# Kernel tuning notes

Measured on AMD Instinct MI355X. Metric: run time of the kernel, lower is better.

## Reference

```python
import jax, jax.numpy as jnp
import numpy as np

B, T, D = 4, 1024, 1024
H, DH = 8, 128           # heads, dim_head = dim // heads
E, FF = 8, 2048          # num_experts, expert hidden_dim
LN_EPS = 1e-5


def setup_inputs() -> dict:
    key = jax.random.key(0)
    ks = jax.random.split(key, 20)
    s = 0.02
    inp = {
        'v': jax.random.normal(ks[0], (B, T, D), jnp.float32),
        'k': jax.random.normal(ks[1], (B, T, D), jnp.float32),
        'q': jax.random.normal(ks[2], (B, T, D), jnp.float32),
        'noise': jax.random.normal(ks[3], (B * T, E), jnp.float32),
        # LayerNorm params (norm_v, norm_k, norm_q, norm_moe, moe output norm)
        'g_v': jnp.ones((D,)), 'b_v': jnp.zeros((D,)),
        'g_k': jnp.ones((D,)), 'b_k': jnp.zeros((D,)),
        'g_q': jnp.ones((D,)), 'b_q': jnp.zeros((D,)),
        'g_moe': jnp.ones((D,)), 'b_moe': jnp.zeros((D,)),
        'g_out': jnp.ones((D,)), 'b_out': jnp.zeros((D,)),
        # LinearAttention projections (q/k/v have no bias, out_proj has bias)
        'Wq': jax.random.normal(ks[4], (D, H * DH), jnp.float32) * s,
        'Wk': jax.random.normal(ks[5], (D, H * DH), jnp.float32) * s,
        'Wv': jax.random.normal(ks[6], (D, H * DH), jnp.float32) * s,
        'Wo': jax.random.normal(ks[7], (H * DH, D), jnp.float32) * s,
        'bo': jnp.zeros((D,)),
        # Router
        'Wr': jax.random.normal(ks[8], (D, E), jnp.float32) * s,
        'br': jnp.zeros((E,)),
        # Experts (stacked): dim -> FF -> dim
        'W1': jax.random.normal(ks[9], (E, D, FF), jnp.float32) * s,
        'b1': jnp.zeros((E, FF)),
        'W2': jax.random.normal(ks[10], (E, FF, D), jnp.float32) * s,
        'b2': jnp.zeros((E, D)),
        'top_k': 2,
    }
    return inp


def _ln(x, g, b):
    mu = x.mean(-1, keepdims=True)
    x0 = x - mu
    var = (x0 * x0).mean(-1, keepdims=True)
    return x0 * jax.lax.rsqrt(var + LN_EPS) * g + b


def reference(v, k, q, noise, g_v, b_v, g_k, b_k, g_q, b_q, g_moe, b_moe,
              g_out, b_out, Wq, Wk, Wv, Wo, bo, Wr, br, W1, b1, W2, b2, top_k):
    # --- LinearAttention over pre-normed v,k,q ---
    qh = jnp.einsum('btd,de->bte', _ln(q, g_q, b_q), Wq).reshape(B, T, H, DH)
    kh = jnp.einsum('btd,de->bte', _ln(k, g_k, b_k), Wk).reshape(B, T, H, DH)
    vh = jnp.einsum('btd,de->bte', _ln(v, g_v, b_v), Wv).reshape(B, T, H, DH)
    qf = jax.nn.elu(qh) + 1.0
    kf = jax.nn.elu(kh) + 1.0
    kv = jnp.einsum('bthd,bthe->bhde', kf, vh)          # [B,H,DH,DH]
    out = jnp.einsum('bthd,bhde->bthe', qf, kv)         # [B,T,H,DH]
    k_sum = kf.sum(axis=1) + 1e-6                       # [B,H,DH]
    denom = jnp.einsum('bthd,bhd->bth', qf, k_sum)[..., None]
    out = out / denom
    attn_out = jnp.einsum('bte,ed->btd', out.reshape(B, T, H * DH), Wo) + bo

    q_res = q + attn_out

    # --- MoEBlock: noisy top-k routing + expert MLPs + residual + LayerNorm ---
    x = _ln(q_res, g_moe, b_moe)
    xf = x.reshape(B * T, D)
    logits = xf @ Wr + br + noise * 0.1                 # noisy gating (randn/10)
    scores = jax.nn.softmax(logits, axis=-1)
    topk_s, topk_i = jax.lax.top_k(scores, top_k)       # [N,K]
    combine = (jax.nn.one_hot(topk_i, E, dtype=scores.dtype) * topk_s[..., None]).sum(1)  # [N,E]
    h = jax.nn.gelu(jnp.einsum('nd,edh->enh', xf, W1) + b1[:, None, :], approximate=False)
    eo = jnp.einsum('enh,ehd->end', h, W2) + b2[:, None, :]
    moe = jnp.einsum('end,ne->nd', eo, combine)         # weighted combine == masked dispatch
    moe_out = _ln(moe.reshape(B, T, D) + x, g_out, b_out)

    return q_res + moe_out
```

## Files before the change

### kernel.cpp

```cpp
#include <hip/hip_runtime.h>
#include <math.h>

typedef __attribute__((ext_vector_type(8))) short short8;
typedef __attribute__((ext_vector_type(4))) float f32x4;

#define LN_EPS 1e-5f

__device__ __forceinline__ float bf2f(unsigned short u) {
  unsigned int x = ((unsigned int)u) << 16;
  float f;
  __builtin_memcpy(&f, &x, 4);
  return f;
}
__device__ __forceinline__ unsigned short f2bf(float f) {
  unsigned int x;
  __builtin_memcpy(&x, &f, 4);
  x += 0x7fffu + ((x >> 16) & 1u);
  return (unsigned short)(x >> 16);
}

__device__ __forceinline__ void gload16(const void* g, void* l) {
  __builtin_amdgcn_global_load_lds(
      (__attribute__((address_space(1))) void*)(void*)g,
      (__attribute__((address_space(3))) void*)l, 16, 0, 0);
}

__device__ __forceinline__ void xcd_swizzle(int& bx, int& by) {
  const int nx = gridDim.x;
  const int nwg = nx * gridDim.y;
  const int orig = blockIdx.y * nx + blockIdx.x;
  const int cpx = nwg >> 3;
  const int lid = (orig & 7) * cpx + (orig >> 3);
  bx = lid % nx;
  by = lid / nx;
}

__device__ __forceinline__ void blockReduce2(float& a, float& b, float* s8) {
#pragma unroll
  for (int off = 32; off > 0; off >>= 1) {
    a += __shfl_down(a, off);
    b += __shfl_down(b, off);
  }
  const int w = threadIdx.x >> 6;
  if ((threadIdx.x & 63) == 0) { s8[w] = a; s8[4 + w] = b; }
  __syncthreads();
  a = s8[0] + s8[1] + s8[2] + s8[3];
  b = s8[4] + s8[5] + s8[6] + s8[7];
}

__global__ __launch_bounds__(256) void ln3_kernel(
    const float* __restrict__ q, const float* __restrict__ k, const float* __restrict__ v,
    const float* __restrict__ gq, const float* __restrict__ bq,
    const float* __restrict__ gk, const float* __restrict__ bk,
    const float* __restrict__ gv, const float* __restrict__ bv,
    unsigned short* __restrict__ oq, unsigned short* __restrict__ ok,
    unsigned short* __restrict__ ov) {
  __shared__ float s8[8];
  const int row = blockIdx.x, which = blockIdx.y;
  const float* x = which == 0 ? q : which == 1 ? k : v;
  const float* g = which == 0 ? gq : which == 1 ? gk : gv;
  const float* b = which == 0 ? bq : which == 1 ? bk : bv;
  unsigned short* o = which == 0 ? oq : which == 1 ? ok : ov;
  const float4 xv = ((const float4*)(x + (size_t)row * 1024))[threadIdx.x];
  float s = xv.x + xv.y + xv.z + xv.w;
  float s2 = xv.x * xv.x + xv.y * xv.y + xv.z * xv.z + xv.w * xv.w;
  blockReduce2(s, s2, s8);
  const float mu = s * (1.f / 1024.f);
  const float rs = rsqrtf(s2 * (1.f / 1024.f) - mu * mu + LN_EPS);
  const int c = threadIdx.x * 4;
  const float y[4] = {xv.x, xv.y, xv.z, xv.w};
#pragma unroll
  for (int j = 0; j < 4; ++j)
    o[(size_t)row * 1024 + c + j] = f2bf((y[j] - mu) * rs * g[c + j] + b[c + j]);
}

__global__ __launch_bounds__(256) void ln_moe_router_kernel(
    const float* __restrict__ qres, const float* __restrict__ g, const float* __restrict__ b,
    const float* __restrict__ Wr, const float* __restrict__ br,
    const float* __restrict__ noise,
    float* __restrict__ xf, unsigned short* __restrict__ xb,
    int* __restrict__ pick, float* __restrict__ pw) {
  __shared__ float s8[8];
  __shared__ float sacc[32];
  const int row = blockIdx.x;
  const float4 xv = ((const float4*)(qres + (size_t)row * 1024))[threadIdx.x];
  float s = xv.x + xv.y + xv.z + xv.w;
  float s2 = xv.x * xv.x + xv.y * xv.y + xv.z * xv.z + xv.w * xv.w;
  blockReduce2(s, s2, s8);
  const float mu = s * (1.f / 1024.f);
  const float rs = rsqrtf(s2 * (1.f / 1024.f) - mu * mu + LN_EPS);
  const int c = threadIdx.x * 4;
  const float yin[4] = {xv.x, xv.y, xv.z, xv.w};
  float y[4];
#pragma unroll
  for (int j = 0; j < 4; ++j) {
    y[j] = (yin[j] - mu) * rs * g[c + j] + b[c + j];
    xf[(size_t)row * 1024 + c + j] = y[j];
    xb[(size_t)row * 1024 + c + j] = f2bf(y[j]);
  }
  float acc[8] = {};
  const float4* wrv = (const float4*)(Wr + (size_t)c * 8);
#pragma unroll
  for (int j = 0; j < 4; ++j) {
    const float4 w0 = wrv[j * 2], w1 = wrv[j * 2 + 1];
    acc[0] += y[j] * w0.x; acc[1] += y[j] * w0.y;
    acc[2] += y[j] * w0.z; acc[3] += y[j] * w0.w;
    acc[4] += y[j] * w1.x; acc[5] += y[j] * w1.y;
    acc[6] += y[j] * w1.z; acc[7] += y[j] * w1.w;
  }
#pragma unroll
  for (int off = 32; off > 0; off >>= 1)
#pragma unroll
    for (int e = 0; e < 8; ++e) acc[e] += __shfl_down(acc[e], off);
  const int w = threadIdx.x >> 6;
  if ((threadIdx.x & 63) == 0)
#pragma unroll
    for (int e = 0; e < 8; ++e) sacc[w * 8 + e] = acc[e];
  __syncthreads();
  if (threadIdx.x == 0) {
    float lg[8], mx = -1e30f;
#pragma unroll
    for (int e = 0; e < 8; ++e) {
      lg[e] = sacc[e] + sacc[8 + e] + sacc[16 + e] + sacc[24 + e] + br[e] +
              0.1f * noise[(size_t)row * 8 + e];
      mx = fmaxf(mx, lg[e]);
    }
    float ssum = 0.f;
#pragma unroll
    for (int e = 0; e < 8; ++e) { lg[e] = expf(lg[e] - mx); ssum += lg[e]; }
    const float inv = 1.f / ssum;
#pragma unroll
    for (int e = 0; e < 8; ++e) lg[e] *= inv;
    int i1 = -1, i2 = -1;
    float m1 = -1.f, m2 = -1.f;
#pragma unroll
    for (int e = 0; e < 8; ++e) {
      if (lg[e] > m1) { m2 = m1; i2 = i1; m1 = lg[e]; i1 = e; }
      else if (lg[e] > m2) { m2 = lg[e]; i2 = e; }
    }
    pick[row * 2] = i1; pick[row * 2 + 1] = i2;
    pw[row * 2] = m1;  pw[row * 2 + 1] = m2;
  }
}

__global__ __launch_bounds__(1024) void route_build_kernel(
    const int* __restrict__ pick, const float* __restrict__ pw,
    int* __restrict__ seg, int* __restrict__ tok, float* __restrict__ wgt,
    int* __restrict__ slt) {
  __shared__ int cnt[8];
  __shared__ int segs[9];
  __shared__ int cur[8];
  const int tid = threadIdx.x;
  if (tid < 8) { cnt[tid] = 0; cur[tid] = 0; }
  __syncthreads();
  for (int i = tid; i < 8192; i += 1024) atomicAdd(&cnt[pick[i]], 1);
  __syncthreads();
  if (tid == 0) {
    int o = 0;
    for (int e = 0; e < 8; ++e) { segs[e] = o; o += (cnt[e] + 127) & ~127; }
    segs[8] = o;
  }
  __syncthreads();
  for (int i = tid; i < 9216; i += 1024) tok[i] = -1;
  if (tid < 9) seg[tid] = segs[tid];
  __syncthreads();
  for (int i = tid; i < 8192; i += 1024) {
    const int n = i >> 1, sl = i & 1;
    const int e = pick[i];
    const int p = atomicAdd(&cur[e], 1);
    const int gr = segs[e] + p;
    tok[gr] = n;
    wgt[gr] = pw[i];
    slt[gr] = sl;
  }
}

__global__ __launch_bounds__(256) void final_kernel(
    const unsigned short* __restrict__ eoSb, const float* __restrict__ xf,
    const float* __restrict__ qres, const float* __restrict__ g,
    const float* __restrict__ b, float* __restrict__ out) {
  __shared__ float s8[8];
  const int row = blockIdx.x;
  const size_t SLOT = (size_t)4096 * 1024;
  const short8 m0v = *(const short8*)(eoSb + (size_t)row * 1024 + threadIdx.x * 4 -
                                      (threadIdx.x * 4 & 7) + ((threadIdx.x & 1) ? 0 : 0));
  const unsigned short* p0 = eoSb + (size_t)row * 1024 + threadIdx.x * 4;
  const unsigned short* p1 = eoSb + SLOT + (size_t)row * 1024 + threadIdx.x * 4;
  const float4 xv = ((const float4*)(xf + (size_t)row * 1024))[threadIdx.x];
  float y[4];
#pragma unroll
  for (int j = 0; j < 4; ++j) y[j] = bf2f(p0[j]) + bf2f(p1[j]);
  y[0] += xv.x; y[1] += xv.y; y[2] += xv.z; y[3] += xv.w;
  float s = y[0] + y[1] + y[2] + y[3];
  float s2 = y[0] * y[0] + y[1] * y[1] + y[2] * y[2] + y[3] * y[3];
  blockReduce2(s, s2, s8);
  const float mu = s * (1.f / 1024.f);
  const float rs = rsqrtf(s2 * (1.f / 1024.f) - mu * mu + LN_EPS);
  const int c = threadIdx.x * 4;
#pragma unroll
  for (int j = 0; j < 4; ++j) {
    const size_t idx = (size_t)row * 1024 + c + j;
    out[idx] = qres[idx] + (y[j] - mu) * rs * g[c + j] + b[c + j];
  }
}

__global__ __launch_bounds__(256) void transposeB_kernel(
    const float* const* __restrict__ ins, unsigned short* const* __restrict__ outs,
    int R, int C) {
  __shared__ float t[32][33];
  const float* inz = ins[blockIdx.z];
  unsigned short* outz = outs[blockIdx.z];
  const int bx = blockIdx.x, by = blockIdx.y;
  const int tx = threadIdx.x & 31, ty = threadIdx.x >> 5;
#pragma unroll
  for (int i = 0; i < 32; i += 8)
    t[ty + i][tx] = inz[(size_t)(by * 32 + ty + i) * C + bx * 32 + tx];
  __syncthreads();
#pragma unroll
  for (int i = 0; i < 32; i += 8)
    outz[(size_t)(bx * 32 + ty + i) * R + by * 32 + tx] = f2bf(t[tx][ty + i]);
}

__global__ __launch_bounds__(256) void transpose8_kernel(
    const float* __restrict__ in, unsigned short* __restrict__ out, int R, int C) {
  __shared__ float t[32][33];
  const float* inz = in + (size_t)blockIdx.z * R * C;
  unsigned short* outz = out + (size_t)blockIdx.z * R * C;
  const int bx = blockIdx.x, by = blockIdx.y;
  const int tx = threadIdx.x & 31, ty = threadIdx.x >> 5;
#pragma unroll
  for (int i = 0; i < 32; i += 8)
    t[ty + i][tx] = inz[(size_t)(by * 32 + ty + i) * C + bx * 32 + tx];
  __syncthreads();
#pragma unroll
  for (int i = 0; i < 32; i += 8)
    outz[(size_t)(bx * 32 + ty + i) * R + by * 32 + tx] = f2bf(t[tx][ty + i]);
}

#define GEMM_STAGE(buf, k0, KD)                                              \
  gload16(gA0 + (k0), lA + (buf) * 4096);                                    \
  gload16(gA1 + (k0), lA + (buf) * 4096 + 16 * 32);                          \
  gload16(gB + (k0), lB + (buf) * 4096);                                     \
  gload16(gB + (size_t)16 * (KD) + (k0), lB + (buf) * 4096 + 16 * 32);

#define GEMM_COMPUTE(buf)                                                    \
  {                                                                          \
    const unsigned short* sA = &As[buf][0];                                  \
    const unsigned short* sB = &Bs[buf][0];                                  \
    short8 af[4], bfr[4];                                                    \
    _Pragma("unroll") for (int m = 0; m < 4; ++m)                            \
        af[m] = *(const short8*)&sA[(arow + m * 16) * 32 + kk];              \
    _Pragma("unroll") for (int n = 0; n < 4; ++n)                            \
        bfr[n] = *(const short8*)&sB[(brow + n * 16) * 32 + kk];             \
    _Pragma("unroll") for (int m = 0; m < 4; ++m)                            \
      _Pragma("unroll") for (int n = 0; n < 4; ++n)                          \
        acc[m][n] = __builtin_amdgcn_mfma_f32_16x16x32_bf16(                 \
            a f[m], bfr[n], acc[m][n], 0, 0, 0);                             \
  }
#undef GEMM_COMPUTE
#define GEMM_COMPUTE(buf)                                                    \
  {                                                                          \
    const unsigned short* sA = &As[buf][0];                                  \
    const unsigned short* sB = &Bs[buf][0];                                  \
    short8 af[4], bfr[4];                                                    \
    _Pragma("unroll") for (int m = 0; m < 4; ++m)                            \
        af[m] = *(const short8*)&sA[(arow + m * 16) * 32 + kk];              \
    _Pragma("unroll") for (int n = 0; n < 4; ++n)                            \
        bfr[n] = *(const short8*)&sB[(brow + n * 16) * 32 + kk];             \
    _Pragma("unroll") for (int m = 0; m < 4; ++m)                            \
      _Pragma("unroll") for (int n = 0; n < 4; ++n)                          \
        acc[m][n] = __builtin_amdgcn_mfma_f32_16x16x32_bf16(                 \
            af[m], bfr[n], acc[m][n], 0, 0, 0);                              \
  }

#define GEMM_LOOP(KD)                                                        \
  GEMM_STAGE(0, 0, KD)                                                       \
  __syncthreads();                                                           \
  for (int k0 = 0; k0 < (KD); k0 += 64) {                                    \
    GEMM_STAGE(1, k0 + 32, KD)                                               \
    GEMM_COMPUTE(0)                                                          \
    __syncthreads();                                                         \
    if (k0 + 64 < (KD)) { GEMM_STAGE(0, k0 + 64, KD) }                       \
    GEMM_COMPUTE(1)                                                          \
    __syncthreads();                                                         \
  }

#define GEMM_PREAMBLE                                                        \
  __shared__ __align__(16) unsigned short As[2][128 * 32];                   \
  __shared__ __align__(16) unsigned short Bs[2][128 * 32];                   \
  const int tid = threadIdx.x;                                               \
  const int lane = tid & 63, w = tid >> 6;                                   \
  const int wr = w >> 1, wc = w & 1;                                         \
  const int sr = lane >> 2, sc = (lane & 3) * 8;                             \
  const int arow = wr * 64 + (lane & 15);                                    \
  const int brow = wc * 64 + (lane & 15);                                    \
  const int kk = (lane >> 4) * 8;                                            \
  unsigned short* lA = &As[0][(w * 32) * 32];                                \
  unsigned short* lB = &Bs[0][(w * 32) * 32];

__global__ __launch_bounds__(256) void gemm_qkv(
    const unsigned short* __restrict__ lnq, const unsigned short* __restrict__ lnk,
    const unsigned short* __restrict__ lnv, const unsigned short* __restrict__ WqT,
    const unsigned short* __restrict__ WkT, const unsigned short* __restrict__ WvT,
    unsigned short* __restrict__ qf, unsigned short* __restrict__ kf,
    unsigned short* __restrict__ vh) {
  const int z = blockIdx.z;
  const unsigned short* A = z == 0 ? lnq : z == 1 ? lnk : lnv;
  const unsigned short* Bt = z == 0 ? WqT : z == 1 ? WkT : WvT;
  unsigned short* outb = z == 0 ? qf : z == 1 ? kf : vh;
  const int K = 1024, N = 1024;
  GEMM_PREAMBLE
  int bx, by;
  xcd_swizzle(bx, by);
  const int row0 = by * 128, col0 = bx * 128;
  const unsigned short* gA0 = A + (size_t)(row0 + w * 32 + sr) * K + sc;
  const unsigned short* gA1 = gA0 + (size_t)16 * K;
  const unsigned short* gB = Bt + (size_t)(col0 + w * 32 + sr) * K + sc;
  f32x4 acc[4][4] = {};
  GEMM_LOOP(1024)
#pragma unroll
  for (int m = 0; m < 4; ++m) {
    const int rbase = row0 + wr * 64 + m * 16 + (lane >> 4) * 4;
#pragma unroll
    for (int n = 0; n < 4; ++n) {
      const int c = col0 + wc * 64 + n * 16 + (lane & 15);
#pragma unroll
      for (int r = 0; r < 4; ++r) {
        float v = acc[m][n][r];
        if (z < 2) v = v > 0.f ? v + 1.f : __expf(v);
        outb[(size_t)(rbase + r) * N + c] = f2bf(v);
      }
    }
  }
}

__global__ __launch_bounds__(256) void gemm_wo(
    const unsigned short* __restrict__ A, const unsigned short* __restrict__ Bt,
    float* __restrict__ outf, const float* __restrict__ bias,
    const float* __restrict__ addm) {
  const int K = 1024, N = 1024;
  GEMM_PREAMBLE
  int bx, by;
  xcd_swizzle(bx, by);
  const int row0 = by * 128, col0 = bx * 128;
  const unsigned short* gA0 = A + (size_t)(row0 + w * 32 + sr) * K + sc;
  const unsigned short* gA1 = gA0 + (size_t)16 * K;
  const unsigned short* gB = Bt + (size_t)(col0 + w * 32 + sr) * K + sc;
  f32x4 acc[4][4] = {};
  GEMM_LOOP(1024)
#pragma unroll
  for (int m = 0; m < 4; ++m) {
    const int rbase = row0 + wr * 64 + m * 16 + (lane >> 4) * 4;
#pragma unroll
    for (int n = 0; n < 4; ++n) {
      const int c = col0 + wc * 64 + n * 16 + (lane & 15);
#pragma unroll
      for (int r = 0; r < 4; ++r) {
        const size_t idx = (size_t)(rbase + r) * N + c;
        outf[idx] = acc[m][n][r] + bias[c] + addm[idx];
      }
    }
  }
}

template <int PHASE>
__global__ __launch_bounds__(256) void gemm_moe(
    const unsigned short* __restrict__ Asrc, const unsigned short* __restrict__ Ball,
    const float* __restrict__ bias_all,
    const int* __restrict__ seg, const int* __restrict__ tok,
    const float* __restrict__ wgt, const int* __restrict__ slt,
    unsigned short* __restrict__ Hb, unsigned short* __restrict__ eoSb) {
  constexpr int K = (PHASE == 1) ? 1024 : 2048;
  constexpr int N = (PHASE == 1) ? 2048 : 1024;
  GEMM_PREAMBLE
  int bx, by;
  xcd_swizzle(bx, by);
  const int row0 = by * 128;
  if (row0 >= seg[8]) return;
  int e = 0;
  while (e < 7 && row0 >= seg[e + 1]) ++e;
  const int col0 = bx * 128;
  const unsigned short* Bt = Ball + (size_t)e * N * K;
  const int gr0 = row0 + w * 32 + sr;
  const int gr1 = gr0 + 16;
  const unsigned short* gA0;
  const unsigned short* gA1;
  if constexpr (PHASE == 1) {
    const int t0 = tok[gr0], t1 = tok[gr1];
    gA0 = Asrc + (size_t)(t0 < 0 ? 0 : t0) * K + sc;
    gA1 = Asrc + (size_t)(t1 < 0 ? 0 : t1) * K + sc;
  } else {
    gA0 = Asrc + (size_t)gr0 * K + sc;
    gA1 = Asrc + (size_t)gr1 * K + sc;
  }
  const unsigned short* gB = Bt + (size_t)(col0 + w * 32 + sr) * K + sc;
  f32x4 acc[4][4] = {};
  if constexpr (PHASE == 1) { GEMM_LOOP(1024) }
  else { GEMM_LOOP(2048) }
  const float* bias = bias_all + (size_t)e * N;
#pragma unroll
  for (int m = 0; m < 4; ++m) {
    const int rloc = wr * 64 + m * 16 + (lane >> 4) * 4;
#pragma unroll
    for (int n = 0; n < 4; ++n) {
      const int c = col0 + wc * 64 + n * 16 + (lane & 15);
#pragma unroll
      for (int r = 0; r < 4; ++r) {
        const int gr = row0 + rloc + r;
        float v = acc[m][n][r] + bias[c];
        if constexpr (PHASE == 1) {
          v = 0.5f * v * (1.f + erff(v * 0.70710678118654752f));
          Hb[(size_t)gr * 2048 + c] = f2bf(v);
        } else {
          const int tkn = tok[gr];
          if (tkn >= 0)
            eoSb[(size_t)slt[gr] * (4096 * 1024) + (size_t)tkn * 1024 + c] =
                f2bf(wgt[gr] * v);
        }
      }
    }
  }
}

__global__ __launch_bounds__(256) void kvpart_kernel(
    const unsigned short* __restrict__ kf, const unsigned short* __restrict__ vh,
    float* __restrict__ kvp, float* __restrict__ ksp) {
  const int bh = blockIdx.x;
  const int b = bh >> 3, h = bh & 7;
  const int ch = blockIdx.y;
  const int tid = threadIdx.x;
  const int d0 = (tid >> 4) * 8, e0 = (tid & 15) * 8;
  __shared__ unsigned short kb[64][128];
  __shared__ unsigned short vb[64][128];
  for (int i = tid; i < 1024; i += 256) {
    const int tt = i >> 4, dd = (i & 15) * 8;
    const size_t base = ((size_t)((b * 1024 + ch * 64 + tt) * 8 + h)) * 128 + dd;
    *(short8*)&kb[tt][dd] = *(const short8*)&kf[base];
    *(short8*)&vb[tt][dd] = *(const short8*)&vh[base];
  }
  __syncthreads();
  float acc[8][8] = {};
  float ks[8] = {};
  for (int tt = 0; tt < 64; ++tt) {
    float kv8[8], vv8[8];
    const short8 kr = *(const short8*)&kb[tt][d0];
    const short8 vr = *(const short8*)&vb[tt][e0];
#pragma unroll
    for (int j = 0; j < 8; ++j) {
      kv8[j] = bf2f((unsigned short)kr[j]);
      vv8[j] = bf2f((unsigned short)vr[j]);
    }
#pragma unroll
    for (int i = 0; i < 8; ++i)
#pragma unroll
      for (int j = 0; j < 8; ++j) acc[i][j] += kv8[i] * vv8[j];
    if ((tid & 15) == 0)
#pragma unroll
      for (int i = 0; i < 8; ++i) ks[i] += kv8[i];
  }
  const size_t obase = ((size_t)(ch * 32 + bh) * 128) * 128;
#pragma unroll
  for (int i = 0; i < 8; ++i)
#pragma unroll
    for (int j = 0; j < 8; ++j)
      kvp[obase + (size_t)(d0 + i) * 128 + e0 + j] = acc[i][j];
  if ((tid & 15) == 0)
#pragma unroll
    for (int i = 0; i < 8; ++i) ksp[(size_t)(ch * 32 + bh) * 128 + d0 + i] = ks[i];
}

__global__ __launch_bounds__(256) void kvreduce_kernel(
    const float* __restrict__ kvp, const float* __restrict__ ksp,
    unsigned short* __restrict__ kvb, float* __restrict__ ksum) {
  const int idx = blockIdx.x * 256 + threadIdx.x;
  const int CS = 32 * 128 * 128;
  float s = 0.f;
#pragma unroll
  for (int c = 0; c < 16; ++c) s += kvp[(size_t)c * CS + idx];
  kvb[idx] = f2bf(s);
  if (idx < 32 * 128) {
    float t = 1e-6f;
#pragma unroll
    for (int c = 0; c < 16; ++c) t += ksp[c * 4096 + idx];
    ksum[idx] = t;
  }
}

__global__ __launch_bounds__(256) void attnout_kernel(
    const unsigned short* __restrict__ qf, const unsigned short* __restrict__ kvb,
    const float* __restrict__ ksum, unsigned short* __restrict__ ctx) {
  const int bh = blockIdx.x, b = bh >> 3, h = bh & 7;
  const int tb = blockIdx.y;
  const int tid = threadIdx.x;
  __shared__ unsigned short kvl[128 * 128];
  __shared__ float ksl[128];
  __shared__ float denom[128];
  __shared__ unsigned short qfl[128 * 32];
  for (int i = tid; i < 16384; i += 256) kvl[i] = kvb[(size_t)bh * 16384 + i];
  if (tid < 128) ksl[tid] = ksum[bh * 128 + tid];
  __syncthreads();
  if (tid < 128) {
    const int t = tb * 128 + tid;
    const size_t qbase = ((size_t)((b * 1024 + t) * 8 + h)) * 128;
    float s = 0.f;
    for (int d = 0; d < 128; ++d) s += bf2f(qf[qbase + d]) * ksl[d];
    denom[tid] = s;
  }
  float acc[8][8] = {};
  const int t0 = (tid >> 4) * 8, e0 = (tid & 15) * 8;
  for (int dc = 0; dc < 128; dc += 32) {
    __syncthreads();
    for (int i = tid; i < 128 * 32; i += 256) {
      const int tt = i >> 5, dd = i & 31;
      qfl[i] = qf[((size_t)((b * 1024 + tb * 128 + tt) * 8 + h)) * 128 + dc + dd];
    }
    __syncthreads();
    for (int dd = 0; dd < 32; ++dd) {
      float kvrow[8];
#pragma unroll
      for (int j = 0; j < 8; ++j) kvrow[j] = bf2f(kvl[(dc + dd) * 128 + e0 + j]);
#pragma unroll
      for (int i = 0; i < 8; ++i) {
        const float qv = bf2f(qfl[(t0 + i) * 32 + dd]);
#pragma unroll
        for (int j = 0; j < 8; ++j) acc[i][j] += qv * kvrow[j];
      }
    }
  }
  __syncthreads();
#pragma unroll
  for (int i = 0; i < 8; ++i) {
    const int t = tb * 128 + t0 + i;
    const float inv = 1.f / denom[t0 + i];
#pragma unroll
    for (int j = 0; j < 8; ++j)
      ctx[((size_t)(b * 1024 + t)) * 1024 + h * 128 + e0 + j] = f2bf(acc[i][j] * inv);
  }
}

__global__ void setptr_kernel(const float* Wq, const float* Wk, const float* Wv,
                              const float* Wo, unsigned short* WqT, unsigned short* WkT,
                              unsigned short* WvT, unsigned short* WoT,
                              const float** ins, unsigned short** outs) {
  if (threadIdx.x == 0) {
    ins[0] = Wq; ins[1] = Wk; ins[2] = Wv; ins[3] = Wo;
    outs[0] = WqT; outs[1] = WkT; outs[2] = WvT; outs[3] = WoT;
  }
}

extern "C" void kernel_launch(void* const* d_in, const int* in_sizes, int n_in,
                              void* d_out, int out_size, void* d_ws, size_t ws_size,
                              hipStream_t stream) {
  (void)in_sizes; (void)n_in; (void)out_size; (void)ws_size;
  const float* vin  = (const float*)d_in[0];
  const float* kin  = (const float*)d_in[1];
  const float* qin  = (const float*)d_in[2];
  const float* noise = (const float*)d_in[3];
  const float* g_v = (const float*)d_in[4];  const float* b_v = (const float*)d_in[5];
  const float* g_k = (const float*)d_in[6];  const float* b_k = (const float*)d_in[7];
  const float* g_q = (const float*)d_in[8];  const float* b_q = (const float*)d_in[9];
  const float* g_moe = (const float*)d_in[10]; const float* b_moe = (const float*)d_in[11];
  const float* g_out = (const float*)d_in[12]; const float* b_out = (const float*)d_in[13];
  const float* Wq = (const float*)d_in[14];
  const float* Wk = (const float*)d_in[15];
  const float* Wv = (const float*)d_in[16];
  const float* Wo = (const float*)d_in[17];
  const float* bo = (const float*)d_in[18];
  const float* Wr = (const float*)d_in[19];
  const float* br = (const float*)d_in[20];
  const float* W1 = (const float*)d_in[21];
  const float* b1 = (const float*)d_in[22];
  const float* W2 = (const float*)d_in[23];
  const float* b2 = (const float*)d_in[24];
  float* out = (float*)d_out;

  const int NT = 4096, D = 1024, FF = 2048;
  const int MAXR = 9216;

  char* p = (char*)d_ws;
  auto alloc = [&](size_t bytes) {
    void* r = (void*)p;
    p += (bytes + 255) & ~(size_t)255;
    return r;
  };
  char* base0 = p;
  unsigned short* lnq = (unsigned short*)alloc((size_t)NT * D * 2);
  unsigned short* lnk = (unsigned short*)alloc((size_t)NT * D * 2);
  unsigned short* lnv = (unsigned short*)alloc((size_t)NT * D * 2);
  unsigned short* WqT = (unsigned short*)alloc((size_t)D * D * 2);
  unsigned short* WkT = (unsigned short*)alloc((size_t)D * D * 2);
  unsigned short* WvT = (unsigned short*)alloc((size_t)D * D * 2);
  unsigned short* WoT = (unsigned short*)alloc((size_t)D * D * 2);
  unsigned short* qf  = (unsigned short*)alloc((size_t)NT * D * 2);
  unsigned short* kf  = (unsigned short*)alloc((size_t)NT * D * 2);
  unsigned short* vh  = (unsigned short*)alloc((size_t)NT * D * 2);
  unsigned short* kvb = (unsigned short*)alloc((size_t)32 * 128 * 128 * 2);
  float* ksp  = (float*)alloc((size_t)16 * 32 * 128 * 4);
  float* ksum = (float*)alloc((size_t)32 * 128 * 4);
  unsigned short* ctx = (unsigned short*)alloc((size_t)NT * D * 2);
  float* qres = (float*)alloc((size_t)NT * D * 4);
  float* xf   = (float*)alloc((size_t)NT * D * 4);
  unsigned short* xb = (unsigned short*)alloc((size_t)NT * D * 2);
  unsigned short* W1T_all = (unsigned short*)alloc((size_t)8 * D * FF * 2);
  unsigned short* W2T_all = (unsigned short*)alloc((size_t)8 * FF * D * 2);
  float* kvp = (float*)alloc((size_t)16 * 32 * 128 * 128 * 4);
  unsigned short* eoSb = (unsigned short*)alloc((size_t)2 * NT * D * 2);
  int* pick = (int*)alloc((size_t)NT * 2 * 4);
  float* pw = (float*)alloc((size_t)NT * 2 * 4);
  int* seg = (int*)alloc(9 * 4);
  int* tokl = (int*)alloc(MAXR * 4);
  float* wgt = (float*)alloc(MAXR * 4);
  int* slt = (int*)alloc(MAXR * 4);
  const float** tins = (const float**)alloc(4 * sizeof(void*));
  unsigned short** touts = (unsigned short**)alloc(4 * sizeof(void*));
  unsigned short* Hb = (unsigned short*)base0;

  setptr_kernel<<<dim3(1), 64, 0, stream>>>(Wq, Wk, Wv, Wo, WqT, WkT, WvT, WoT,
                                            tins, touts);
  transposeB_kernel<<<dim3(32, 32, 4), 256, 0, stream>>>(tins, touts, D, D);

  ln3_kernel<<<dim3(NT, 3), 256, 0, stream>>>(qin, kin, vin, g_q, b_q, g_k, b_k, g_v, b_v,
                                              lnq, lnk, lnv);

  gemm_qkv<<<dim3(D / 128, NT / 128, 3), 256, 0, stream>>>(lnq, lnk, lnv, WqT, WkT, WvT,
                                                           qf, kf, vh);

  kvpart_kernel<<<dim3(32, 16), 256, 0, stream>>>(kf, vh, kvp, ksp);
  kvreduce_kernel<<<dim3(2048), 256, 0, stream>>>(kvp, ksp, kvb, ksum);
  attnout_kernel<<<dim3(32, 8), 256, 0, stream>>>(qf, kvb, ksum, ctx);

  gemm_wo<<<dim3(D / 128, NT / 128), 256, 0, stream>>>(ctx, WoT, qres, bo, qin);

  ln_moe_router_kernel<<<dim3(NT), 256, 0, stream>>>(qres, g_moe, b_moe, Wr, br, noise,
                                                     xf, xb, pick, pw);
  route_build_kernel<<<dim3(1), 1024, 0, stream>>>(pick, pw, seg, tokl, wgt, slt);

  transpose8_kernel<<<dim3(FF / 32, D / 32, 8), 256, 0, stream>>>(W1, W1T_all, D, FF);
  transpose8_kernel<<<dim3(D / 32, FF / 32, 8), 256, 0, stream>>>(W2, W2T_all, FF, D);

  gemm_moe<1><<<dim3(FF / 128, MAXR / 128), 256, 0, stream>>>(
      xb, W1T_all, b1, seg, tokl, wgt, slt, Hb, nullptr);
  gemm_moe<2><<<dim3(D / 128, MAXR / 128), 256, 0, stream>>>(
      Hb, W2T_all, b2, seg, tokl, wgt, slt, nullptr, eoSb);

  final_kernel<<<dim3(NT), 256, 0, stream>>>(eoSb, xf, qres, g_out, b_out, out);
}
```

Measured before the change: 387.8 us.

## Widen QKV and MoE GEMM tiles to 128x256 with 512-thread blocks

Introduces a new GEMM template with 8 waves per block computing a 128x256 output tile, and uses it for the QKV projection and both MoE expert GEMMs. Each A tile loaded into LDS is now reused across twice as many output columns, which cuts global and LDS traffic per FLOP. It also removes a dead load in final_kernel and a duplicate macro definition. The cost is a larger LDS footprint, half as many blocks (which lowers occupancy and parallelism on the many-CU device), and more wasted work on partially filled MoE segments.

New measurement: 402.2 us. +3.7%, slower.

```diff
diff --git a/kernel.cpp b/kernel.cpp
--- a/kernel.cpp
+++ b/kernel.cpp
@@ -182,8 +182,6 @@
   __shared__ float s8[8];
   const int row = blockIdx.x;
   const size_t SLOT = (size_t)4096 * 1024;
-  const short8 m0v = *(const short8*)(eoSb + (size_t)row * 1024 + threadIdx.x * 4 -
-                                      (threadIdx.x * 4 & 7) + ((threadIdx.x & 1) ? 0 : 0));
   const unsigned short* p0 = eoSb + (size_t)row * 1024 + threadIdx.x * 4;
   const unsigned short* p1 = eoSb + SLOT + (size_t)row * 1024 + threadIdx.x * 4;
   const float4 xv = ((const float4*)(xf + (size_t)row * 1024))[threadIdx.x];
@@ -243,21 +241,6 @@
   gload16(gB + (k0), lB + (buf) * 4096);                                     \
   gload16(gB + (size_t)16 * (KD) + (k0), lB + (buf) * 4096 + 16 * 32);
 
-#define GEMM_COMPUTE(buf)                                                    \
-  {                                                                          \
-    const unsigned short* sA = &As[buf][0];                                  \
-    const unsigned short* sB = &Bs[buf][0];                                  \
-    short8 af[4], bfr[4];                                                    \
-    _Pragma("unroll") for (int m = 0; m < 4; ++m)                            \
-        af[m] = *(const short8*)&sA[(arow + m * 16) * 32 + kk];              \
-    _Pragma("unroll") for (int n = 0; n < 4; ++n)                            \
-        bfr[n] = *(const short8*)&sB[(brow + n * 16) * 32 + kk];             \
-    _Pragma("unroll") for (int m = 0; m < 4; ++m)                            \
-      _Pragma("unroll") for (int n = 0; n < 4; ++n)                          \
-        acc[m][n] = __builtin_amdgcn_mfma_f32_16x16x32_bf16(                 \
-            a f[m], bfr[n], acc[m][n], 0, 0, 0);                             \
-  }
-#undef GEMM_COMPUTE
 #define GEMM_COMPUTE(buf)                                                    \
   {                                                                          \
     const unsigned short* sA = &As[buf][0];                                  \
@@ -297,42 +280,6 @@
   const int kk = (lane >> 4) * 8;                                            \
   unsigned short* lA = &As[0][(w * 32) * 32];                                \
   unsigned short* lB = &Bs[0][(w * 32) * 32];
-
-__global__ __launch_bounds__(256) void gemm_qkv(
-    const unsigned short* __restrict__ lnq, const unsigned short* __restrict__ lnk,
-    const unsigned short* __restrict__ lnv, const unsigned short* __restrict__ WqT,
-    const unsigned short* __restrict__ WkT, const unsigned short* __restrict__ WvT,
-    unsigned short* __restrict__ qf, unsigned short* __restrict__ kf,
-    unsigned short* __restrict__ vh) {
-  const int z = blockIdx.z;
-  const unsigned short* A = z == 0 ? lnq : z == 1 ? lnk : lnv;
-  const unsigned short* Bt = z == 0 ? WqT : z == 1 ? WkT : WvT;
-  unsigned short* outb = z == 0 ? qf : z == 1 ? kf : vh;
-  const int K = 1024, N = 1024;
-  GEMM_PREAMBLE
-  int bx, by;
-  xcd_swizzle(bx, by);
-  const int row0 = by * 128, col0 = bx * 128;
-  const unsigned short* gA0 = A + (size_t)(row0 + w * 32 + sr) * K + sc;
-  const unsigned short* gA1 = gA0 + (size_t)16 * K;
-  const unsigned short* gB = Bt + (size_t)(col0 + w * 32 + sr) * K + sc;
-  f32x4 acc[4][4] = {};
-  GEMM_LOOP(1024)
-#pragma unroll
-  for (int m = 0; m < 4; ++m) {
-    const int rbase = row0 + wr * 64 + m * 16 + (lane >> 4) * 4;
-#pragma unroll
-    for (int n = 0; n < 4; ++n) {
-      const int c = col0 + wc * 64 + n * 16 + (lane & 15);
-#pragma unroll
-      for (int r = 0; r < 4; ++r) {
-        float v = acc[m][n][r];
-        if (z < 2) v = v > 0.f ? v + 1.f : __expf(v);
-        outb[(size_t)(rbase + r) * N + c] = f2bf(v);
-      }
-    }
-  }
-}
 
 __global__ __launch_bounds__(256) void gemm_wo(
     const unsigned short* __restrict__ A, const unsigned short* __restrict__ Bt,
@@ -363,8 +310,88 @@
   }
 }
 
+#define G2_PREAMBLE                                                          \
+  __shared__ __align__(16) unsigned short As[2][128 * 32];                   \
+  __shared__ __align__(16) unsigned short Bs[2][256 * 32];                   \
+  const int tid = threadIdx.x;                                               \
+  const int lane = tid & 63, w = tid >> 6;                                   \
+  const int wr = w >> 2, wc = w & 3;                                         \
+  const int arow = wr * 64 + (lane & 15);                                    \
+  const int brow = wc * 64 + (lane & 15);                                    \
+  const int kk = (lane >> 4) * 8;                                            \
+  char* lA = (char*)&As[0][0] + w * 1024;                                    \
+  char* lB = (char*)&Bs[0][0] + w * 1024;
+
+#define G2_STAGE(buf, k0)                                                    \
+  gload16(gA + (k0), lA + (buf) * 8192);                                     \
+  gload16(gB0 + (k0), lB + (buf) * 16384);                                   \
+  gload16(gB1 + (k0), lB + (buf) * 16384 + 8192);
+
+#define G2_COMPUTE(buf)                                                      \
+  {                                                                          \
+    const unsigned short* sA = &As[buf][0];                                  \
+    const unsigned short* sB = &Bs[buf][0];                                  \
+    short8 af[4], bfr[4];                                                    \
+    _Pragma("unroll") for (int m = 0; m < 4; ++m)                            \
+        af[m] = *(const short8*)&sA[(arow + m * 16) * 32 + kk];              \
+    _Pragma("unroll") for (int n = 0; n < 4; ++n)                            \
+        bfr[n] = *(const short8*)&sB[(brow + n * 16) * 32 + kk];             \
+    _Pragma("unroll") for (int m = 0; m < 4; ++m)                            \
+      _Pragma("unroll") for (int n = 0; n < 4; ++n)                          \
+        acc[m][n] = __builtin_amdgcn_mfma_f32_16x16x32_bf16(                 \
+            af[m], bfr[n], acc[m][n], 0, 0, 0);                              \
+  }
+
+#define G2_LOOP(KD)                                                          \
+  G2_STAGE(0, 0)                                                             \
+  __syncthreads();                                                           \
+  for (int k0 = 0; k0 < (KD); k0 += 64) {                                    \
+    G2_STAGE(1, k0 + 32)                                                     \
+    G2_COMPUTE(0)                                                            \
+    __syncthreads();                                                         \
+    if (k0 + 64 < (KD)) { G2_STAGE(0, k0 + 64) }                             \
+    G2_COMPUTE(1)                                                            \
+    __syncthreads();                                                         \
+  }
+
+__global__ __launch_bounds__(512) void gemm_qkv(
+    const unsigned short* __restrict__ lnq, const unsigned short* __restrict__ lnk,
+    const unsigned short* __restrict__ lnv, const unsigned short* __restrict__ WqT,
+    const unsigned short* __restrict__ WkT, const unsigned short* __restrict__ WvT,
+    unsigned short* __restrict__ qf, unsigned short* __restrict__ kf,
+    unsigned short* __restrict__ vh) {
+  const int z = blockIdx.z;
+  const unsigned short* A = z == 0 ? lnq : z == 1 ? lnk : lnv;
+  const unsigned short* Bt = z == 0 ? WqT : z == 1 ? WkT : WvT;
+  unsigned short* outb = z == 0 ? qf : z == 1 ? kf : vh;
+  const int K = 1024, N = 1024;
+  G2_PREAMBLE
+  int bx, by;
+  xcd_swizzle(bx, by);
+  const int row0 = by * 128, col0 = bx * 256;
+  const unsigned short* gA = A + (size_t)(row0 + (tid >> 2)) * K + (tid & 3) * 8;
+  const unsigned short* gB0 = Bt + (size_t)(col0 + (tid >> 2)) * K + (tid & 3) * 8;
+  const unsigned short* gB1 = Bt + (size_t)(col0 + 128 + (tid >> 2)) * K + (tid & 3) * 8;
+  f32x4 acc[4][4] = {};
+  G2_LOOP(1024)
+#pragma unroll
+  for (int m = 0; m < 4; ++m) {
+    const int rbase = row0 + wr * 64 + m * 16 + (lane >> 4) * 4;
+#pragma unroll
+    for (int n = 0; n < 4; ++n) {
+      const int c = col0 + wc * 64 + n * 16 + (lane & 15);
+#pragma unroll
+      for (int r = 0; r < 4; ++r) {
+        float v = acc[m][n][r];
+        if (z < 2) v = v > 0.f ? v + 1.f : __expf(v);
+        outb[(size_t)(rbase + r) * N + c] = f2bf(v);
+      }
+    }
+  }
+}
+
 template <int PHASE>
-__global__ __launch_bounds__(256) void gemm_moe(
+__global__ __launch_bounds__(512) void gemm_moe(
     const unsigned short* __restrict__ Asrc, const unsigned short* __restrict__ Ball,
     const float* __restrict__ bias_all,
     const int* __restrict__ seg, const int* __restrict__ tok,
@@ -372,31 +399,27 @@
     unsigned short* __restrict__ Hb, unsigned short* __restrict__ eoSb) {
   constexpr int K = (PHASE == 1) ? 1024 : 2048;
   constexpr int N = (PHASE == 1) ? 2048 : 1024;
-  GEMM_PREAMBLE
+  G2_PREAMBLE
   int bx, by;
   xcd_swizzle(bx, by);
   const int row0 = by * 128;
   if (row0 >= seg[8]) return;
   int e = 0;
   while (e < 7 && row0 >= seg[e + 1]) ++e;
-  const int col0 = bx * 128;
+  const int col0 = bx * 256;
   const unsigned short* Bt = Ball + (size_t)e * N * K;
-  const int gr0 = row0 + w * 32 + sr;
-  const int gr1 = gr0 + 16;
-  const unsigned short* gA0;
-  const unsigned short* gA1;
+  const unsigned short* gA;
   if constexpr (PHASE == 1) {
-    const int t0 = tok[gr0], t1 = tok[gr1];
-    gA0 = Asrc + (size_t)(t0 < 0 ? 0 : t0) * K + sc;
-    gA1 = Asrc + (size_t)(t1 < 0 ? 0 : t1) * K + sc;
+    const int t0 = tok[row0 + (tid >> 2)];
+    gA = Asrc + (size_t)(t0 < 0 ? 0 : t0) * K + (tid & 3) * 8;
   } else {
-    gA0 = Asrc + (size_t)gr0 * K + sc;
-    gA1 = Asrc + (size_t)gr1 * K + sc;
-  }
-  const unsigned short* gB = Bt + (size_t)(col0 + w * 32 + sr) * K + sc;
+    gA = Asrc + (size_t)(row0 + (tid >> 2)) * K + (tid & 3) * 8;
+  }
+  const unsigned short* gB0 = Bt + (size_t)(col0 + (tid >> 2)) * K + (tid & 3) * 8;
+  const unsigned short* gB1 = Bt + (size_t)(col0 + 128 + (tid >> 2)) * K + (tid & 3) * 8;
   f32x4 acc[4][4] = {};
-  if constexpr (PHASE == 1) { GEMM_LOOP(1024) }
-  else { GEMM_LOOP(2048) }
+  if constexpr (PHASE == 1) { G2_LOOP(1024) }
+  else { G2_LOOP(2048) }
   const float* bias = bias_all + (size_t)e * N;
 #pragma unroll
   for (int m = 0; m < 4; ++m) {
@@ -622,7 +645,7 @@
   ln3_kernel<<<dim3(NT, 3), 256, 0, stream>>>(qin, kin, vin, g_q, b_q, g_k, b_k, g_v, b_v,
                                               lnq, lnk, lnv);
 
-  gemm_qkv<<<dim3(D / 128, NT / 128, 3), 256, 0, stream>>>(lnq, lnk, lnv, WqT, WkT, WvT,
+  gemm_qkv<<<dim3(D / 256, NT / 128, 3), 512, 0, stream>>>(lnq, lnk, lnv, WqT, WkT, WvT,
                                                            qf, kf, vh);
 
   kvpart_kernel<<<dim3(32, 16), 256, 0, stream>>>(kf, vh, kvp, ksp);
@@ -638,9 +661,9 @@
   transpose8_kernel<<<dim3(FF / 32, D / 32, 8), 256, 0, stream>>>(W1, W1T_all, D, FF);
   transpose8_kernel<<<dim3(D / 32, FF / 32, 8), 256, 0, stream>>>(W2, W2T_all, FF, D);
 
-  gemm_moe<1><<<dim3(FF / 128, MAXR / 128), 256, 0, stream>>>(
+  gemm_moe<1><<<dim3(FF / 256, MAXR / 128), 512, 0, stream>>>(
       xb, W1T_all, b1, seg, tokl, wgt, slt, Hb, nullptr);
-  gemm_moe<2><<<dim3(D / 128, MAXR / 128), 256, 0, stream>>>(
+  gemm_moe<2><<<dim3(D / 256, MAXR / 128), 512, 0, stream>>>(
       Hb, W2T_all, b2, seg, tokl, wgt, slt, nullptr, eoSb);
 
   final_kernel<<<dim3(NT), 256, 0, stream>>>(eoSb, xf, qres, g_out, b_out, out);
```

## Swizzle GEMM LDS layout to avoid bank conflicts and store KV partials in bf16

Applied to the files above, without the earlier changes.

Applies an XOR swizzle to the column chunk used when staging A/B tiles into LDS and when reading MFMA fragments, aiming to remove LDS bank conflicts in all GEMMs built from the shared macros. It also stores the per-chunk KV partial sums as bf16 instead of fp32, halving the partial-buffer traffic between kvpart and kvreduce. It removes a dead load and a duplicated macro definition as well. The bf16 partials add rounding error before the 16-way reduction.

After: 377.8 us. -2.6%, faster.

```diff
diff --git a/kernel.cpp b/kernel.cpp
--- a/kernel.cpp
+++ b/kernel.cpp
@@ -182,8 +182,6 @@
   __shared__ float s8[8];
   const int row = blockIdx.x;
   const size_t SLOT = (size_t)4096 * 1024;
-  const short8 m0v = *(const short8*)(eoSb + (size_t)row * 1024 + threadIdx.x * 4 -
-                                      (threadIdx.x * 4 & 7) + ((threadIdx.x & 1) ? 0 : 0));
   const unsigned short* p0 = eoSb + (size_t)row * 1024 + threadIdx.x * 4;
   const unsigned short* p1 = eoSb + SLOT + (size_t)row * 1024 + threadIdx.x * 4;
   const float4 xv = ((const float4*)(xf + (size_t)row * 1024))[threadIdx.x];
@@ -249,24 +247,9 @@
     const unsigned short* sB = &Bs[buf][0];                                  \
     short8 af[4], bfr[4];                                                    \
     _Pragma("unroll") for (int m = 0; m < 4; ++m)                            \
-        af[m] = *(const short8*)&sA[(arow + m * 16) * 32 + kk];              \
+        af[m] = *(const short8*)&sA[(arow + m * 16) * 32 + kksw];            \
     _Pragma("unroll") for (int n = 0; n < 4; ++n)                            \
-        bfr[n] = *(const short8*)&sB[(brow + n * 16) * 32 + kk];             \
-    _Pragma("unroll") for (int m = 0; m < 4; ++m)                            \
-      _Pragma("unroll") for (int n = 0; n < 4; ++n)                          \
-        acc[m][n] = __builtin_amdgcn_mfma_f32_16x16x32_bf16(                 \
-            a f[m], bfr[n], acc[m][n], 0, 0, 0);                             \
-  }
-#undef GEMM_COMPUTE
-#define GEMM_COMPUTE(buf)                                                    \
-  {                                                                          \
-    const unsigned short* sA = &As[buf][0];                                  \
-    const unsigned short* sB = &Bs[buf][0];                                  \
-    short8 af[4], bfr[4];                                                    \
-    _Pragma("unroll") for (int m = 0; m < 4; ++m)                            \
-        af[m] = *(const short8*)&sA[(arow + m * 16) * 32 + kk];              \
-    _Pragma("unroll") for (int n = 0; n < 4; ++n)                            \
-        bfr[n] = *(const short8*)&sB[(brow + n * 16) * 32 + kk];             \
+        bfr[n] = *(const short8*)&sB[(brow + n * 16) * 32 + kksw];           \
     _Pragma("unroll") for (int m = 0; m < 4; ++m)                            \
       _Pragma("unroll") for (int n = 0; n < 4; ++n)                          \
         acc[m][n] = __builtin_amdgcn_mfma_f32_16x16x32_bf16(                 \
@@ -291,10 +274,11 @@
   const int tid = threadIdx.x;                                               \
   const int lane = tid & 63, w = tid >> 6;                                   \
   const int wr = w >> 1, wc = w & 1;                                         \
-  const int sr = lane >> 2, sc = (lane & 3) * 8;                             \
+  const int sr = lane >> 2;                                                  \
+  const int sc = (((lane & 3) ^ ((lane >> 3) & 3)) * 8);   \
   const int arow = wr * 64 + (lane & 15);                                    \
   const int brow = wc * 64 + (lane & 15);                                    \
-  const int kk = (lane >> 4) * 8;                                            \
+  const int kksw = (((lane >> 4) ^ ((lane >> 1) & 3)) * 8);    \
   unsigned short* lA = &As[0][(w * 32) * 32];                                \
   unsigned short* lB = &Bs[0][(w * 32) * 32];
 
@@ -424,7 +408,7 @@
 
 __global__ __launch_bounds__(256) void kvpart_kernel(
     const unsigned short* __restrict__ kf, const unsigned short* __restrict__ vh,
-    float* __restrict__ kvp, float* __restrict__ ksp) {
+    unsigned short* __restrict__ kvp, float* __restrict__ ksp) {
   const int bh = blockIdx.x;
   const int b = bh >> 3, h = bh & 7;
   const int ch = blockIdx.y;
@@ -463,20 +447,20 @@
   for (int i = 0; i < 8; ++i)
 #pragma unroll
     for (int j = 0; j < 8; ++j)
-      kvp[obase + (size_t)(d0 + i) * 128 + e0 + j] = acc[i][j];
+      kvp[obase + (size_t)(d0 + i) * 128 + e0 + j] = f2bf(acc[i][j]);
   if ((tid & 15) == 0)
 #pragma unroll
     for (int i = 0; i < 8; ++i) ksp[(size_t)(ch * 32 + bh) * 128 + d0 + i] = ks[i];
 }
 
 __global__ __launch_bounds__(256) void kvreduce_kernel(
-    const float* __restrict__ kvp, const float* __restrict__ ksp,
+    const unsigned short* __restrict__ kvp, const float* __restrict__ ksp,
     unsigned short* __restrict__ kvb, float* __restrict__ ksum) {
   const int idx = blockIdx.x * 256 + threadIdx.x;
   const int CS = 32 * 128 * 128;
   float s = 0.f;
 #pragma unroll
-  for (int c = 0; c < 16; ++c) s += kvp[(size_t)c * CS + idx];
+  for (int c = 0; c < 16; ++c) s += bf2f(kvp[(size_t)c * CS + idx]);
   kvb[idx] = f2bf(s);
   if (idx < 32 * 128) {
     float t = 1e-6f;
@@ -603,7 +587,7 @@
   unsigned short* xb = (unsigned short*)alloc((size_t)NT * D * 2);
   unsigned short* W1T_all = (unsigned short*)alloc((size_t)8 * D * FF * 2);
   unsigned short* W2T_all = (unsigned short*)alloc((size_t)8 * FF * D * 2);
-  float* kvp = (float*)alloc((size_t)16 * 32 * 128 * 128 * 4);
+  unsigned short* kvp = (unsigned short*)alloc((size_t)16 * 32 * 128 * 128 * 2);
   unsigned short* eoSb = (unsigned short*)alloc((size_t)2 * NT * D * 2);
   int* pick = (int*)alloc((size_t)NT * 2 * 4);
   float* pw = (float*)alloc((size_t)NT * 2 * 4);
```
